# Kernel optimization log

Hardware: AMD Instinct MI355X
Metric: run time of the kernel (lower is better)

Reference implementation:

```python
import jax, jax.numpy as jnp
import numpy as np
import math

B, S, D, H, F = 2, 2048, 1024, 16, 4096
HD = D // H

def _xavier(key, fan_in, fan_out):
    limit = math.sqrt(6.0 / (fan_in + fan_out))
    return jax.random.uniform(key, (fan_in, fan_out), jnp.float32, -limit, limit)

def setup_inputs() -> dict:
    key = jax.random.key(0)
    ks = jax.random.split(key, 8)
    inp = {
        'x': jax.random.normal(ks[0], (B, S, D), jnp.float32),
        # attention projections (stored [in, out]; biases zero-init per module)
        'Wq': _xavier(ks[1], D, D), 'bq': jnp.zeros((D,), jnp.float32),
        'Wk': _xavier(ks[2], D, D), 'bk': jnp.zeros((D,), jnp.float32),
        'Wv': _xavier(ks[3], D, D), 'bv': jnp.zeros((D,), jnp.float32),
        'Wp': _xavier(ks[4], D, D), 'bp': jnp.zeros((D,), jnp.float32),
        # layer norms
        'g1': jnp.ones((D,), jnp.float32), 'be1': jnp.zeros((D,), jnp.float32),
        'g2': jnp.ones((D,), jnp.float32), 'be2': jnp.zeros((D,), jnp.float32),
        # feed-forward
        'W1': _xavier(ks[5], D, F), 'bf1': jnp.zeros((F,), jnp.float32),
        'W2': _xavier(ks[6], F, D), 'bf2': jnp.zeros((D,), jnp.float32),
    }
    return inp

def _layernorm(x, g, b, eps=1e-5):
    mu = jnp.mean(x, axis=-1, keepdims=True)
    var = jnp.var(x, axis=-1, keepdims=True)
    return (x - mu) * jax.lax.rsqrt(var + eps) * g + b

def _block(x, Wq, bq, Wk, bk, Wv, bv, Wp, bp, g1, be1, g2, be2, W1, bf1, W2, bf2):
    b, s, d = x.shape
    # --- pre-LN attention ---
    a_in = _layernorm(x, g1, be1)
    q = (a_in @ Wq + bq).reshape(b, s, H, HD).transpose(0, 2, 1, 3)  # [B,H,S,HD]
    k = (a_in @ Wk + bk).reshape(b, s, H, HD).transpose(0, 2, 1, 3)
    v = (a_in @ Wv + bv).reshape(b, s, H, HD).transpose(0, 2, 1, 3)
    scores = jnp.einsum('bhqd,bhkd->bhqk', q, k) / math.sqrt(HD)
    causal = jnp.tril(jnp.ones((s, s), dtype=bool))
    scores = jnp.where(causal, scores, -jnp.inf)
    attn = jax.nn.softmax(scores, axis=-1)
    out = jnp.einsum('bhqk,bhkd->bhqd', attn, v)
    out = out.transpose(0, 2, 1, 3).reshape(b, s, d)
    x = x + (out @ Wp + bp)
    # --- pre-LN feed-forward ---
    f_in = _layernorm(x, g2, be2)
    h = jax.nn.gelu(f_in @ W1 + bf1, approximate=False)
    x = x + (h @ W2 + bf2)
    return x

def reference(x, Wq, bq, Wk, bk, Wv, bv, Wp, bp, g1, be1, g2, be2, W1, bf1, W2, bf2):
    return _block(x, Wq, bq, Wk, bk, Wv, bv, Wp, bp, g1, be1, g2, be2, W1, bf1, W2, bf2)
```

## Files before the change

kernel.cpp:

```cpp
#include <hip/hip_runtime.h>
#include <hip/hip_bf16.h>

#define AS1 __attribute__((address_space(1)))
#define AS3 __attribute__((address_space(3)))

typedef __bf16 bf16;
typedef __attribute__((ext_vector_type(8))) __bf16 bf16x8;
typedef __attribute__((ext_vector_type(4))) __bf16 bf16x4;
typedef __attribute__((ext_vector_type(4))) float f32x4;

#define NB 2
#define NS 2048
#define ND 1024
#define NH 16
#define NF 4096
#define NHD 64
#define NM (NB*NS)

__device__ __forceinline__ void gload16(const void* g, void* l) {
  __builtin_amdgcn_global_load_lds((AS1 void*)g, (AS3 void*)l, 16, 0, 0);
}

__global__ void tb_wtrans_all(const float* __restrict__ Wq, const float* __restrict__ Wk,
                              const float* __restrict__ Wv, const float* __restrict__ Wp,
                              const float* __restrict__ W1, const float* __restrict__ W2,
                              bf16* __restrict__ WqT, bf16* __restrict__ WkT,
                              bf16* __restrict__ WvT, bf16* __restrict__ WpT,
                              bf16* __restrict__ W1T, bf16* __restrict__ W2T) {
  __shared__ float t[64][65];
  const int bid = blockIdx.x;
  const float* W; bf16* Wt; int K, N, nb, kb;
  if (bid < 1024) {
    const int z = bid >> 8, i = bid & 255;
    K = ND; N = ND; nb = (i & 15) << 6; kb = (i >> 4) << 6;
    W  = (z == 0) ? Wq  : (z == 1) ? Wk  : (z == 2) ? Wv  : Wp;
    Wt = (z == 0) ? WqT : (z == 1) ? WkT : (z == 2) ? WvT : WpT;
  } else if (bid < 2048) {
    const int i = bid - 1024;
    K = ND; N = NF; nb = (i & 63) << 6; kb = (i >> 6) << 6;
    W = W1; Wt = W1T;
  } else {
    const int i = bid - 2048;
    K = NF; N = ND; nb = (i & 15) << 6; kb = (i >> 4) << 6;
    W = W2; Wt = W2T;
  }
  const int tid = threadIdx.x;
#pragma unroll
  for (int i = 0; i < 16; ++i) {
    const int lin = tid + (i << 8);
    const int r = lin >> 6, c = lin & 63;
    t[r][c] = W[(size_t)(kb + r) * N + nb + c];
  }
  __syncthreads();
#pragma unroll
  for (int i = 0; i < 16; ++i) {
    const int lin = tid + (i << 8);
    const int r = lin >> 6, c = lin & 63;
    Wt[(size_t)(nb + r) * K + kb + c] = (bf16)t[c][r];
  }
}

__global__ void tb_vtrans(const bf16* __restrict__ v, bf16* __restrict__ vt) {
  __shared__ bf16 t[64][72];
  const int bh = blockIdx.y;
  const int sb = blockIdx.x << 6;
  const int tid = threadIdx.x;
  const bf16* src = v + ((size_t)bh * NS + sb) * NHD;
  bf16* dst = vt + (size_t)bh * NHD * NS + sb;
  const int r = tid >> 3;
  const int c8 = (tid & 7) << 3;
#pragma unroll
  for (int i = 0; i < 2; ++i) {
    const int row = r + i * 32;
    const bf16x8 xv = *(const bf16x8*)(src + (size_t)row * NHD + c8);
#pragma unroll
    for (int j = 0; j < 8; ++j) t[row][c8 + j] = xv[j];
  }
  __syncthreads();
#pragma unroll
  for (int i = 0; i < 2; ++i) {
    const int row = r + i * 32;
    bf16x8 ov;
#pragma unroll
    for (int j = 0; j < 8; ++j) ov[j] = t[c8 + j][row];
    *(bf16x8*)(dst + (size_t)row * NS + c8) = ov;
  }
}

__global__ void tb_lnorm(const float* __restrict__ xin, const float* __restrict__ g,
                         const float* __restrict__ be, bf16* __restrict__ outp) {
  const int row = blockIdx.x;
  const int tid = threadIdx.x;
  const float4 v = ((const float4*)(xin + (size_t)row * ND))[tid];
  float s  = v.x + v.y + v.z + v.w;
  float ss = v.x*v.x + v.y*v.y + v.z*v.z + v.w*v.w;
#pragma unroll
  for (int off = 32; off; off >>= 1) {
    s  += __shfl_xor(s,  off, 64);
    ss += __shfl_xor(ss, off, 64);
  }
  __shared__ float red[8];
  const int lane = tid & 63, wv = tid >> 6;
  if (lane == 0) { red[wv] = s; red[4 + wv] = ss; }
  __syncthreads();
  s  = red[0] + red[1] + red[2] + red[3];
  ss = red[4] + red[5] + red[6] + red[7];
  const float mu = s * (1.0f / ND);
  const float var = ss * (1.0f / ND) - mu * mu;
  const float rstd = rsqrtf(var + 1e-5f);
  const float4 gv = ((const float4*)g)[tid];
  const float4 bv = ((const float4*)be)[tid];
  bf16x4 o;
  o[0] = (bf16)((v.x - mu) * rstd * gv.x + bv.x);
  o[1] = (bf16)((v.y - mu) * rstd * gv.y + bv.y);
  o[2] = (bf16)((v.z - mu) * rstd * gv.z + bv.z);
  o[3] = (bf16)((v.w - mu) * rstd * gv.w + bv.w);
  ((bf16x4*)(outp + (size_t)row * ND))[tid] = o;
}

template <int MODE>
__global__ void __launch_bounds__(256, 2)
tb_gemm(const bf16* __restrict__ A,
        const bf16* __restrict__ B0, const bf16* __restrict__ B1, const bf16* __restrict__ B2,
        const float* __restrict__ bias0, const float* __restrict__ bias1, const float* __restrict__ bias2,
        void* __restrict__ o0, void* __restrict__ o1, void* __restrict__ o2,
        int Ktot) {
  __shared__ __align__(16) bf16 As[128 * 64];
  __shared__ __align__(16) bf16 Bs[128 * 64];
  const bf16* Bt = B0; const float* bias = bias0; void* outp = o0;
  if (MODE == 0) {
    if (blockIdx.z == 1)      { Bt = B1; bias = bias1; outp = o1; }
    else if (blockIdx.z == 2) { Bt = B2; bias = bias2; outp = o2; }
  }
  const int tid = threadIdx.x;
  const int lane = tid & 63, wv = tid >> 6;
  const int wr = wv >> 1, wc = wv & 1;
  const int m0 = blockIdx.y * 128, n0 = blockIdx.x * 128;

  f32x4 acc[4][4] = {};

  const int srow = (wv << 3) + (lane >> 3);
  const int scb  = ((lane & 7) << 4);

  for (int k0 = 0; k0 < Ktot; k0 += 64) {
    __syncthreads();
#pragma unroll
    for (int i = 0; i < 4; ++i) {
      const int row = i * 32 + srow;
      const int cb = scb ^ ((row & 7) << 4);
      gload16(A  + (size_t)(m0 + row) * Ktot + k0 + (cb >> 1), (char*)As + i * 4096 + wv * 1024);
      gload16(Bt + (size_t)(n0 + row) * Ktot + k0 + (cb >> 1), (char*)Bs + i * 4096 + wv * 1024);
    }
    __syncthreads();
#pragma unroll
    for (int kk = 0; kk < 2; ++kk) {
      bf16x8 af[4], bfr[4];
#pragma unroll
      for (int mi = 0; mi < 4; ++mi) {
        const int row = wr * 64 + mi * 16 + (lane & 15);
        const int cb = (kk * 64 + ((lane >> 4) << 4)) ^ ((row & 7) << 4);
        af[mi] = *(const bf16x8*)((const char*)As + row * 128 + cb);
      }
#pragma unroll
      for (int ni = 0; ni < 4; ++ni) {
        const int row = wc * 64 + ni * 16 + (lane & 15);
        const int cb = (kk * 64 + ((lane >> 4) << 4)) ^ ((row & 7) << 4);
        bfr[ni] = *(const bf16x8*)((const char*)Bs + row * 128 + cb);
      }
#pragma unroll
      for (int mi = 0; mi < 4; ++mi)
#pragma unroll
        for (int ni = 0; ni < 4; ++ni)
          acc[mi][ni] = __builtin_amdgcn_mfma_f32_16x16x32_bf16(af[mi], bfr[ni], acc[mi][ni], 0, 0, 0);
    }
  }
#pragma unroll
  for (int mi = 0; mi < 4; ++mi) {
#pragma unroll
    for (int ni = 0; ni < 4; ++ni) {
      const int rbase = m0 + wr * 64 + mi * 16 + ((lane >> 4) << 2);
      const int gcol  = n0 + wc * 64 + ni * 16 + (lane & 15);
#pragma unroll
      for (int r = 0; r < 4; ++r) {
        const int grow = rbase + r;
        const float val = acc[mi][ni][r] + bias[gcol];
        if (MODE == 0) {
          const int b = grow >> 11, sIdx = grow & 2047;
          const int h = gcol >> 6, hd = gcol & 63;
          ((bf16*)outp)[(((size_t)(b * NH + h)) * NS + sIdx) * NHD + hd] = (bf16)val;
        } else {
          const float gelu = 0.5f * val * (1.0f + erff(val * 0.70710678f));
          ((bf16*)outp)[(size_t)grow * NF + gcol] = (bf16)gelu;
        }
      }
    }
  }
}

__global__ void __launch_bounds__(256, 2)
tb_gemm64(const bf16* __restrict__ A, const bf16* __restrict__ Bt,
          const float* __restrict__ bias, const float* __restrict__ resid,
          float* __restrict__ outp, int Ktot) {
  __shared__ __align__(16) bf16 As[2][64 * 64];
  __shared__ __align__(16) bf16 Bs[2][128 * 64];
  const int bid = blockIdx.x;
  const int xcd = bid & 7, j = bid >> 3;
  const int m0 = (xcd * 8 + (j & 7)) * 64;
  const int n0 = (j >> 3) * 128;
  const int tid = threadIdx.x;
  const int lane = tid & 63, wv = tid >> 6;
  const int wr = wv >> 1, wc = wv & 1;

  f32x4 acc[2][4] = {};

  const int srow = (wv << 3) + (lane >> 3);
  const int scb  = ((lane & 7) << 4);
  const int NT = Ktot >> 6;

#define GSTAGE64(buf, t_) do {                                                 \
    _Pragma("unroll")                                                          \
    for (int i_ = 0; i_ < 2; ++i_) {                                           \
      const int row_ = i_ * 32 + srow;                                         \
      const int cb_ = scb ^ ((row_ & 7) << 4);                                 \
      gload16(A + (size_t)(m0 + row_) * Ktot + ((t_) << 6) + (cb_ >> 1),       \
              (char*)As[buf] + i_ * 4096 + wv * 1024);                         \
    }                                                                          \
    _Pragma("unroll")                                                          \
    for (int i_ = 0; i_ < 4; ++i_) {                                           \
      const int row_ = i_ * 32 + srow;                                         \
      const int cb_ = scb ^ ((row_ & 7) << 4);                                 \
      gload16(Bt + (size_t)(n0 + row_) * Ktot + ((t_) << 6) + (cb_ >> 1),      \
              (char*)Bs[buf] + i_ * 4096 + wv * 1024);                         \
    } } while (0)

  GSTAGE64(0, 0);
  asm volatile("s_waitcnt vmcnt(0)" ::: "memory");
  __builtin_amdgcn_s_barrier();

  for (int t = 0; t < NT; ++t) {
    const int cur = t & 1;
    if (t + 1 < NT) GSTAGE64(cur ^ 1, t + 1);
    const char* Ab = (const char*)As[cur];
    const char* Bb = (const char*)Bs[cur];
#pragma unroll
    for (int kk = 0; kk < 2; ++kk) {
      bf16x8 af[2], bfr[4];
#pragma unroll
      for (int mi = 0; mi < 2; ++mi) {
        const int row = wr * 32 + mi * 16 + (lane & 15);
        const int cb = (kk * 64 + ((lane >> 4) << 4)) ^ ((row & 7) << 4);
        af[mi] = *(const bf16x8*)(Ab + row * 128 + cb);
      }
#pragma unroll
      for (int ni = 0; ni < 4; ++ni) {
        const int row = wc * 64 + ni * 16 + (lane & 15);
        const int cb = (kk * 64 + ((lane >> 4) << 4)) ^ ((row & 7) << 4);
        bfr[ni] = *(const bf16x8*)(Bb + row * 128 + cb);
      }
#pragma unroll
      for (int mi = 0; mi < 2; ++mi)
#pragma unroll
        for (int ni = 0; ni < 4; ++ni)
          acc[mi][ni] = __builtin_amdgcn_mfma_f32_16x16x32_bf16(af[mi], bfr[ni], acc[mi][ni], 0, 0, 0);
    }
    if (t + 1 < NT) {
      asm volatile("s_waitcnt vmcnt(0)" ::: "memory");
      __builtin_amdgcn_s_barrier();
    }
  }
#undef GSTAGE64

#pragma unroll
  for (int mi = 0; mi < 2; ++mi) {
#pragma unroll
    for (int ni = 0; ni < 4; ++ni) {
      const int rbase = m0 + wr * 32 + mi * 16 + ((lane >> 4) << 2);
      const int gcol  = n0 + wc * 64 + ni * 16 + (lane & 15);
#pragma unroll
      for (int r = 0; r < 4; ++r) {
        const size_t idx = (size_t)(rbase + r) * ND + gcol;
        outp[idx] = resid[idx] + acc[mi][ni][r] + bias[gcol];
      }
    }
  }
}

__global__ void __launch_bounds__(256, 4)
tb_attn(const bf16* __restrict__ qg, const bf16* __restrict__ kg,
        const bf16* __restrict__ vtg, bf16* __restrict__ og) {
  __shared__ __align__(16) bf16 Ks[2][64 * 64];
  __shared__ __align__(16) bf16 Vts[2][64 * 64];
  __shared__ __align__(16) bf16 Ps[4][16 * 64];
  const int bid = blockIdx.x;
  const int u = bid & 255, v = bid >> 8;
  const int bh = u & 31;
  const int s = ((u >> 5) << 2) + v;
  const int qt = (s & 1) ? (31 - (s >> 1)) : (s >> 1);
  const int tid = threadIdx.x;
  const int lane = tid & 63, wv = tid >> 6;
  const bf16* Qp  = qg  + (size_t)bh * NS * NHD;
  const bf16* Kp  = kg  + (size_t)bh * NS * NHD;
  const bf16* Vtp = vtg + (size_t)bh * NHD * NS;
  char* const Pw = (char*)&Ps[wv][0];
  const int qbase = qt * 64 + wv * 16;

  bf16x8 qa[2];
#pragma unroll
  for (int kk = 0; kk < 2; ++kk)
    qa[kk] = *(const bf16x8*)(Qp + (size_t)(qbase + (lane & 15)) * NHD
                              + kk * 32 + ((lane >> 4) << 3));

  f32x4 Of[4] = {};
  float mrow[4], lrow[4];
#pragma unroll
  for (int r = 0; r < 4; ++r) { mrow[r] = -1e30f; lrow[r] = 0.0f; }

  const int srow = (wv << 3) + (lane >> 3);
  const int scb  = (lane & 7) << 4;
  const int nkb = qt + 1;

#define STAGE_KV(buf, kbi_) do {                                               \
    _Pragma("unroll")                                                          \
    for (int i_ = 0; i_ < 2; ++i_) {                                           \
      const int row_ = i_ * 32 + srow;                                         \
      const int cb_ = scb ^ ((row_ & 7) << 4);                                 \
      gload16(Kp  + (size_t)((kbi_) * 64 + row_) * NHD + (cb_ >> 1),           \
              (char*)Ks[buf] + i_ * 4096 + wv * 1024);                         \
      gload16(Vtp + (size_t)row_ * NS + (kbi_) * 64 + (cb_ >> 1),              \
              (char*)Vts[buf] + i_ * 4096 + wv * 1024);                        \
    } } while (0)

  STAGE_KV(0, 0);
  __syncthreads();

  for (int kbi = 0; kbi < nkb; ++kbi) {
    const int cur = kbi & 1;
    if (kbi + 1 < nkb) STAGE_KV(cur ^ 1, kbi + 1);
    const bool maskedT = (kbi == qt);

    f32x4 sf[4] = {};
#pragma unroll
    for (int kk = 0; kk < 2; ++kk) {
#pragma unroll
      for (int f = 0; f < 4; ++f) {
        const int row = f * 16 + (lane & 15);
        const int cb = (kk * 64 + ((lane >> 4) << 4)) ^ ((row & 7) << 4);
        const bf16x8 kf = *(const bf16x8*)((const char*)Ks[cur] + row * 128 + cb);
        sf[f] = __builtin_amdgcn_mfma_f32_16x16x32_bf16(qa[kk], kf, sf[f], 0, 0, 0);
      }
    }

    float tmax[4];
#pragma unroll
    for (int r = 0; r < 4; ++r) tmax[r] = -1e30f;
#pragma unroll
    for (int f = 0; f < 4; ++f)
#pragma unroll
      for (int r = 0; r < 4; ++r) {
        float sv = sf[f][r] * 0.125f;
        if (maskedT) {
          const int kcol = kbi * 64 + f * 16 + (lane & 15);
          const int qrow = qbase + ((lane >> 4) << 2) + r;
          sv = (kcol <= qrow) ? sv : -1e30f;
        }
        sf[f][r] = sv;
        tmax[r] = fmaxf(tmax[r], sv);
      }
#pragma unroll
    for (int off = 8; off; off >>= 1)
#pragma unroll
      for (int r = 0; r < 4; ++r)
        tmax[r] = fmaxf(tmax[r], __shfl_xor(tmax[r], off, 64));
#pragma unroll
    for (int r = 0; r < 4; ++r) {
      const float mnew = fmaxf(mrow[r], tmax[r]);
      const float alpha = __expf(mrow[r] - mnew);
      mrow[r] = mnew;
      float ps = 0.0f;
#pragma unroll
      for (int f = 0; f < 4; ++f) {
        const float p = __expf(sf[f][r] - mnew);
        sf[f][r] = p;
        ps += p;
      }
      lrow[r] = lrow[r] * alpha + ps;
#pragma unroll
      for (int hf = 0; hf < 4; ++hf) Of[hf][r] *= alpha;
    }

#pragma unroll
    for (int f = 0; f < 4; ++f) {
      const int col = f * 16 + (lane & 15);
#pragma unroll
      for (int r = 0; r < 4; ++r) {
        const int prow = ((lane >> 4) << 2) + r;
        *(bf16*)(Pw + prow * 128 + ((col * 2) ^ ((prow & 7) << 4))) = (bf16)sf[f][r];
      }
    }

#pragma unroll
    for (int kk = 0; kk < 2; ++kk) {
      const int prow = lane & 15;
      const int pcb = (kk * 64 + ((lane >> 4) << 4)) ^ ((prow & 7) << 4);
      const bf16x8 pa = *(const bf16x8*)(Pw + prow * 128 + pcb);
#pragma unroll
      for (int hf = 0; hf < 4; ++hf) {
        const int vrow = hf * 16 + (lane & 15);
        const int vcb = (kk * 64 + ((lane >> 4) << 4)) ^ ((vrow & 7) << 4);
        const bf16x8 vbf = *(const bf16x8*)((const char*)Vts[cur] + vrow * 128 + vcb);
        Of[hf] = __builtin_amdgcn_mfma_f32_16x16x32_bf16(pa, vbf, Of[hf], 0, 0, 0);
      }
    }
    __syncthreads();
  }
#undef STAGE_KV

#pragma unroll
  for (int off = 8; off; off >>= 1)
#pragma unroll
    for (int r = 0; r < 4; ++r)
      lrow[r] += __shfl_xor(lrow[r], off, 64);
  const int b = bh >> 4, h = bh & 15;
#pragma unroll
  for (int r = 0; r < 4; ++r) {
    const float inv = 1.0f / lrow[r];
    const int q = qbase + ((lane >> 4) << 2) + r;
    bf16* dst = og + ((size_t)b * NS + q) * ND + h * NHD;
#pragma unroll
    for (int hf = 0; hf < 4; ++hf)
      dst[hf * 16 + (lane & 15)] = (bf16)(Of[hf][r] * inv);
  }
}

extern "C" void kernel_launch(void* const* d_in, const int* in_sizes, int n_in,
                              void* d_out, int out_size, void* d_ws, size_t ws_size,
                              hipStream_t stream) {
  (void)in_sizes; (void)n_in; (void)out_size; (void)ws_size;
  const float* x   = (const float*)d_in[0];
  const float* Wq  = (const float*)d_in[1];
  const float* bq  = (const float*)d_in[2];
  const float* Wk  = (const float*)d_in[3];
  const float* bk  = (const float*)d_in[4];
  const float* Wv  = (const float*)d_in[5];
  const float* bv  = (const float*)d_in[6];
  const float* Wp  = (const float*)d_in[7];
  const float* bp  = (const float*)d_in[8];
  const float* g1  = (const float*)d_in[9];
  const float* be1 = (const float*)d_in[10];
  const float* g2  = (const float*)d_in[11];
  const float* be2 = (const float*)d_in[12];
  const float* W1  = (const float*)d_in[13];
  const float* bf1 = (const float*)d_in[14];
  const float* W2  = (const float*)d_in[15];
  const float* bf2 = (const float*)d_in[16];
  float* outp = (float*)d_out;

  char* w = (char*)d_ws;
  bf16* WqT  = (bf16*)(w + (0u  << 20));
  bf16* WkT  = (bf16*)(w + (2u  << 20));
  bf16* WvT  = (bf16*)(w + (4u  << 20));
  bf16* WpT  = (bf16*)(w + (6u  << 20));
  bf16* W1T  = (bf16*)(w + (8u  << 20));
  bf16* W2T  = (bf16*)(w + (16u << 20));
  bf16* Abuf = (bf16*)(w + (24u << 20));
  bf16* vt   = (bf16*)(w + (24u << 20));
  bf16* qb   = (bf16*)(w + (32u << 20));
  bf16* kb   = (bf16*)(w + (40u << 20));
  bf16* vb   = (bf16*)(w + (48u << 20));
  bf16* ao   = (bf16*)(w + (56u << 20));
  bf16* hb   = (bf16*)(w + (32u << 20));
  float* x2  = outp;

  tb_wtrans_all<<<3072, 256, 0, stream>>>(Wq, Wk, Wv, Wp, W1, W2,
                                          WqT, WkT, WvT, WpT, W1T, W2T);

  tb_lnorm<<<NM, 256, 0, stream>>>(x, g1, be1, Abuf);
  tb_gemm<0><<<dim3(8, 32, 3), 256, 0, stream>>>(Abuf, WqT, WkT, WvT, bq, bk, bv,
                                                 qb, kb, vb, ND);
  tb_vtrans<<<dim3(32, 32), 256, 0, stream>>>(vb, vt);
  tb_attn<<<1024, 256, 0, stream>>>(qb, kb, vt, ao);
  tb_gemm64<<<512, 256, 0, stream>>>(ao, WpT, bp, x, x2, ND);
  tb_lnorm<<<NM, 256, 0, stream>>>(x2, g2, be2, Abuf);
  tb_gemm<2><<<dim3(32, 32, 1), 256, 0, stream>>>(Abuf, W1T, W1T, W1T, bf1, bf1, bf1,
                                                  hb, hb, hb, ND);
  tb_gemm64<<<512, 256, 0, stream>>>(hb, W2T, bf2, x2, outp, NF);
}
```

Before: 250.4 us.

## Split long causal attention query tiles across two KV-range blocks with combine kernel

```diff
diff --git a/kernel.cpp b/kernel.cpp
--- a/kernel.cpp
+++ b/kernel.cpp
@@ -16,6 +16,9 @@
 #define NF 4096
 #define NHD 64
 #define NM (NB*NS)
+
+#define PSLOT 8704
+#define QSPLIT 18
 
 __device__ __forceinline__ void gload16(const void* g, void* l) {
   __builtin_amdgcn_global_load_lds((AS1 void*)g, (AS3 void*)l, 16, 0, 0);
@@ -287,15 +290,28 @@
 
 __global__ void __launch_bounds__(256, 4)
 tb_attn(const bf16* __restrict__ qg, const bf16* __restrict__ kg,
-        const bf16* __restrict__ vtg, bf16* __restrict__ og) {
+        const bf16* __restrict__ vtg, bf16* __restrict__ og,
+        char* __restrict__ part) {
   __shared__ __align__(16) bf16 Ks[2][64 * 64];
   __shared__ __align__(16) bf16 Vts[2][64 * 64];
   __shared__ __align__(16) bf16 Ps[4][16 * 64];
   const int bid = blockIdx.x;
-  const int u = bid & 255, v = bid >> 8;
-  const int bh = u & 31;
-  const int s = ((u >> 5) << 2) + v;
-  const int qt = (s & 1) ? (31 - (s >> 1)) : (s >> 1);
+  const int u = bid >> 5, bh = bid & 31;
+  int qt, kv0, kv1, slot = 0;
+  bool is_split;
+  if (u < 28) {
+    is_split = true;
+    qt = 31 - (u >> 1);
+    const int sp = u & 1;
+    const int half = (qt + 1) >> 1;
+    kv0 = sp ? half : 0;
+    kv1 = sp ? (qt + 1) : half;
+    slot = ((bh * 14 + (qt - QSPLIT)) << 1) + sp;
+  } else {
+    is_split = false;
+    qt = 45 - u;
+    kv0 = 0; kv1 = qt + 1;
+  }
   const int tid = threadIdx.x;
   const int lane = tid & 63, wv = tid >> 6;
   const bf16* Qp  = qg  + (size_t)bh * NS * NHD;
@@ -317,7 +333,6 @@
 
   const int srow = (wv << 3) + (lane >> 3);
   const int scb  = (lane & 7) << 4;
-  const int nkb = qt + 1;
 
 #define STAGE_KV(buf, kbi_) do {                                               \
     _Pragma("unroll")                                                          \
@@ -330,12 +345,12 @@
               (char*)Vts[buf] + i_ * 4096 + wv * 1024);                        \
     } } while (0)
 
-  STAGE_KV(0, 0);
+  STAGE_KV(0, kv0);
   __syncthreads();
 
-  for (int kbi = 0; kbi < nkb; ++kbi) {
-    const int cur = kbi & 1;
-    if (kbi + 1 < nkb) STAGE_KV(cur ^ 1, kbi + 1);
+  for (int kbi = kv0; kbi < kv1; ++kbi) {
+    const int cur = (kbi - kv0) & 1;
+    if (kbi + 1 < kv1) STAGE_KV(cur ^ 1, kbi + 1);
     const bool maskedT = (kbi == qt);
 
     f32x4 sf[4] = {};
@@ -420,15 +435,61 @@
 #pragma unroll
     for (int r = 0; r < 4; ++r)
       lrow[r] += __shfl_xor(lrow[r], off, 64);
+
+  if (!is_split) {
+    const int b = bh >> 4, h = bh & 15;
+#pragma unroll
+    for (int r = 0; r < 4; ++r) {
+      const float inv = 1.0f / lrow[r];
+      const int q = qbase + ((lane >> 4) << 2) + r;
+      bf16* dst = og + ((size_t)b * NS + q) * ND + h * NHD;
+#pragma unroll
+      for (int hf = 0; hf < 4; ++hf)
+        dst[hf * 16 + (lane & 15)] = (bf16)(Of[hf][r] * inv);
+    }
+  } else {
+    char* const P = part + (size_t)slot * PSLOT;
+    bf16* const PO = (bf16*)P;
+    float* const ml = (float*)(P + 8192);
+#pragma unroll
+    for (int r = 0; r < 4; ++r) {
+      const int row = wv * 16 + ((lane >> 4) << 2) + r;
+#pragma unroll
+      for (int hf = 0; hf < 4; ++hf)
+        PO[row * 64 + hf * 16 + (lane & 15)] = (bf16)Of[hf][r];
+      if ((lane & 15) == 0) {
+        ml[row * 2]     = mrow[r];
+        ml[row * 2 + 1] = lrow[r];
+      }
+    }
+  }
+}
+
+__global__ void tb_comb(const char* __restrict__ part, bf16* __restrict__ og) {
+  const int qt = QSPLIT + blockIdx.x;
+  const int bh = blockIdx.y;
+  const int tid = threadIdx.x;
+  const int row = tid >> 2, c0 = (tid & 3) << 4;
+  const char* P0 = part + (size_t)(((bh * 14 + (qt - QSPLIT)) << 1) + 0) * PSLOT;
+  const char* P1 = P0 + PSLOT;
+  const float2 ml0 = ((const float2*)(P0 + 8192))[row];
+  const float2 ml1 = ((const float2*)(P1 + 8192))[row];
+  const float m = fmaxf(ml0.x, ml1.x);
+  const float w0 = __expf(ml0.x - m), w1 = __expf(ml1.x - m);
+  const float inv = 1.0f / (w0 * ml0.y + w1 * ml1.y);
+  const bf16* O0 = (const bf16*)P0 + row * 64 + c0;
+  const bf16* O1 = (const bf16*)P1 + row * 64 + c0;
   const int b = bh >> 4, h = bh & 15;
-#pragma unroll
-  for (int r = 0; r < 4; ++r) {
-    const float inv = 1.0f / lrow[r];
-    const int q = qbase + ((lane >> 4) << 2) + r;
-    bf16* dst = og + ((size_t)b * NS + q) * ND + h * NHD;
-#pragma unroll
-    for (int hf = 0; hf < 4; ++hf)
-      dst[hf * 16 + (lane & 15)] = (bf16)(Of[hf][r] * inv);
+  bf16* dst = og + ((size_t)b * NS + qt * 64 + row) * ND + h * NHD + c0;
+#pragma unroll
+  for (int half = 0; half < 2; ++half) {
+    const bf16x8 a = *(const bf16x8*)(O0 + half * 8);
+    const bf16x8 c = *(const bf16x8*)(O1 + half * 8);
+    bf16x8 o;
+#pragma unroll
+    for (int j = 0; j < 8; ++j)
+      o[j] = (bf16)((w0 * (float)a[j] + w1 * (float)c[j]) * inv);
+    *(bf16x8*)(dst + half * 8) = o;
   }
 }
 
@@ -467,6 +528,7 @@
   bf16* qb   = (bf16*)(w + (32u << 20));
   bf16* kb   = (bf16*)(w + (40u << 20));
   bf16* vb   = (bf16*)(w + (48u << 20));
+  char* part = (char*)(w + (48u << 20));
   bf16* ao   = (bf16*)(w + (56u << 20));
   bf16* hb   = (bf16*)(w + (32u << 20));
   float* x2  = outp;
@@ -478,7 +540,8 @@
   tb_gemm<0><<<dim3(8, 32, 3), 256, 0, stream>>>(Abuf, WqT, WkT, WvT, bq, bk, bv,
                                                  qb, kb, vb, ND);
   tb_vtrans<<<dim3(32, 32), 256, 0, stream>>>(vb, vt);
-  tb_attn<<<1024, 256, 0, stream>>>(qb, kb, vt, ao);
+  tb_attn<<<1472, 256, 0, stream>>>(qb, kb, vt, ao, part);
+  tb_comb<<<dim3(14, 32), 256, 0, stream>>>(part, ao);
   tb_gemm64<<<512, 256, 0, stream>>>(ao, WpT, bp, x, x2, ND);
   tb_lnorm<<<NM, 256, 0, stream>>>(x2, g2, be2, Abuf);
   tb_gemm<2><<<dim3(32, 32, 1), 256, 0, stream>>>(Abuf, W1T, W1T, W1T, bf1, bf1, bf1,
```

Result: slower. 256.9 us (+2.6%).

## Use split-K GEMM with atomic accumulation for the FFN down projection

Applied to the files above, without the earlier changes.

```diff
diff --git a/kernel.cpp b/kernel.cpp
--- a/kernel.cpp
+++ b/kernel.cpp
@@ -286,6 +286,75 @@
 }
 
 __global__ void __launch_bounds__(256, 4)
+tb_gemmsk(const bf16* __restrict__ A, const bf16* __restrict__ Bt,
+          const float* __restrict__ bias, float* __restrict__ outp) {
+  __shared__ __align__(16) bf16 As[128 * 64];
+  __shared__ __align__(16) bf16 Bs[128 * 64];
+  const int bid = blockIdx.x;
+  const int xcd = bid & 7, j = bid >> 3;
+  const int m0 = (xcd * 4 + (j & 3)) * 128;
+  const int n0 = ((j >> 2) & 7) * 128;
+  const int z  = j >> 5;
+  const int tid = threadIdx.x;
+  const int lane = tid & 63, wv = tid >> 6;
+  const int wr = wv >> 1, wc = wv & 1;
+
+  f32x4 acc[4][4] = {};
+
+  const int srow = (wv << 3) + (lane >> 3);
+  const int scb  = ((lane & 7) << 4);
+  const int kbase = z * (NF / 4);
+
+  for (int t = 0; t < 16; ++t) {
+    const int k0 = kbase + t * 64;
+    __syncthreads();
+#pragma unroll
+    for (int i = 0; i < 4; ++i) {
+      const int row = i * 32 + srow;
+      const int cb = scb ^ ((row & 7) << 4);
+      gload16(A  + (size_t)(m0 + row) * NF + k0 + (cb >> 1), (char*)As + i * 4096 + wv * 1024);
+      gload16(Bt + (size_t)(n0 + row) * NF + k0 + (cb >> 1), (char*)Bs + i * 4096 + wv * 1024);
+    }
+    __syncthreads();
+#pragma unroll
+    for (int kk = 0; kk < 2; ++kk) {
+      bf16x8 af[4], bfr[4];
+#pragma unroll
+      for (int mi = 0; mi < 4; ++mi) {
+        const int row = wr * 64 + mi * 16 + (lane & 15);
+        const int cb = (kk * 64 + ((lane >> 4) << 4)) ^ ((row & 7) << 4);
+        af[mi] = *(const bf16x8*)((const char*)As + row * 128 + cb);
+      }
+#pragma unroll
+      for (int ni = 0; ni < 4; ++ni) {
+        const int row = wc * 64 + ni * 16 + (lane & 15);
+        const int cb = (kk * 64 + ((lane >> 4) << 4)) ^ ((row & 7) << 4);
+        bfr[ni] = *(const bf16x8*)((const char*)Bs + row * 128 + cb);
+      }
+#pragma unroll
+      for (int mi = 0; mi < 4; ++mi)
+#pragma unroll
+        for (int ni = 0; ni < 4; ++ni)
+          acc[mi][ni] = __builtin_amdgcn_mfma_f32_16x16x32_bf16(af[mi], bfr[ni], acc[mi][ni], 0, 0, 0);
+    }
+  }
+#pragma unroll
+  for (int mi = 0; mi < 4; ++mi) {
+#pragma unroll
+    for (int ni = 0; ni < 4; ++ni) {
+      const int rbase = m0 + wr * 64 + mi * 16 + ((lane >> 4) << 2);
+      const int gcol  = n0 + wc * 64 + ni * 16 + (lane & 15);
+      const float bz = (z == 0) ? bias[gcol] : 0.0f;
+#pragma unroll
+      for (int r = 0; r < 4; ++r) {
+        const size_t idx = (size_t)(rbase + r) * ND + gcol;
+        atomicAdd(outp + idx, acc[mi][ni][r] + bz);
+      }
+    }
+  }
+}
+
+__global__ void __launch_bounds__(256, 4)
 tb_attn(const bf16* __restrict__ qg, const bf16* __restrict__ kg,
         const bf16* __restrict__ vtg, bf16* __restrict__ og) {
   __shared__ __align__(16) bf16 Ks[2][64 * 64];
@@ -483,5 +552,5 @@
   tb_lnorm<<<NM, 256, 0, stream>>>(x2, g2, be2, Abuf);
   tb_gemm<2><<<dim3(32, 32, 1), 256, 0, stream>>>(Abuf, W1T, W1T, W1T, bf1, bf1, bf1,
                                                   hb, hb, hb, ND);
-  tb_gemm64<<<512, 256, 0, stream>>>(hb, W2T, bf2, x2, outp, NF);
-}
+  tb_gemmsk<<<1024, 256, 0, stream>>>(hb, W2T, bf2, outp);
+}
```

New measurement: 266.3 us. 1.06x slower.
